# Optimization experiments

Measured on AMD Instinct MI355X. Metric: run time of the kernel, lower is better.

Reference implementation:

```python
import jax, jax.numpy as jnp
import numpy as np

N_U = 8192
N_C = 8192
D_IN = 32
D_HID = 32  # hidden_dim == output_dim (required by the concat->Linear shape)


def _glorot(key, fan_in, fan_out):
    r = np.sqrt(6.0 / (fan_in + fan_out)).astype(np.float32)
    return jax.random.uniform(key, (fan_in, fan_out), jnp.float32, -r, r)


def setup_inputs() -> dict:
    key = jax.random.key(0)
    ks = jax.random.split(key, 12)
    X_U = jax.random.normal(ks[0], (N_U, D_IN), jnp.float32)
    X_C = jax.random.normal(ks[1], (N_C, D_IN), jnp.float32)
    adj_uu = jax.random.uniform(ks[2], (N_U, N_U), jnp.float32)
    adj_uc = jax.random.uniform(ks[3], (N_U, N_C), jnp.float32)
    adj_cc = jax.random.uniform(ks[4], (N_C, N_C), jnp.float32)
    weight_s = _glorot(ks[5], D_IN, D_HID)          # GCN_S.weight (shared for uu and cc)
    proj_u = _glorot(ks[6], D_IN, D_HID)            # GCN_C.projection_u
    proj_c = _glorot(ks[7], D_IN, D_HID)            # GCN_C.projection_c (unused in fwd math)
    weight_c = _glorot(ks[8], D_HID, D_HID)         # GCN_C.weight
    W_lin = jax.random.normal(ks[9], (D_IN + D_HID, D_HID), jnp.float32) * 0.05  # Linear, no bias
    a_vec = jax.random.normal(ks[10], (D_HID, 1), jnp.float32) * 0.05            # attention vector
    return {"X_U": X_U, "X_C": X_C, "adj_uu": adj_uu, "adj_uc": adj_uc, "adj_cc": adj_cc,
            "weight_s": weight_s, "proj_u": proj_u, "proj_c": proj_c,
            "weight_c": weight_c, "W_lin": W_lin, "a_vec": a_vec}


def gcn_s(adj, x, w):
    # D^-1/2 A D^-1/2 (X W), with D = 1 + rowsum(A); expressed as broadcast scaling
    dinv = jax.lax.rsqrt(1.0 + jnp.sum(adj, axis=1))  # [N]
    support = x @ w                                    # [N, d]
    return dinv[:, None] * (adj @ (dinv[:, None] * support))


def gcn_c(adj, x_u, p_u, w):
    # Du^-1/2 A Dc^-1/2 ((X_U P_u) W); projected_c is computed but unused upstream
    du = jax.lax.rsqrt(jnp.sum(adj, axis=1))  # [N_u]
    dc = jax.lax.rsqrt(jnp.sum(adj, axis=0))  # [N_c]
    support = (x_u @ p_u) @ w                  # [N_u, d]
    return du[:, None] * (adj @ (dc[:, None] * support))  # wait: see note below


def gcn_c_correct(adj, x_u, p_u, w):
    # norm_adj = diag(du) @ adj @ diag(dc)  -> [N_u, N_c]; output = norm_adj @ support ([N_u,d])
    # Actually original multiplies [N_u,N_c] norm_adj by support built from X_U [N_u,d]:
    # this only typechecks when N_u == N_c (as in the repo's usage). We keep that math.
    du = jax.lax.rsqrt(jnp.sum(adj, axis=1))
    dc = jax.lax.rsqrt(jnp.sum(adj, axis=0))
    support = (x_u @ p_u) @ w
    return du[:, None] * (adj @ (dc[:, None] * support))


def reference(X_U, X_C, adj_uu, adj_uc, adj_cc, weight_s, proj_u, proj_c, weight_c, W_lin, a_vec):
    node_embed_u = gcn_s(adj_uu, X_U, weight_s)            # [N_u, d]
    node_embed_c1 = gcn_s(adj_cc, X_C, weight_s)           # [N_c, d]
    node_embed_c2 = gcn_c_correct(adj_uc, X_U, proj_u, weight_c)  # [N_c, d]

    a_tau_1 = jax.nn.relu(jnp.concatenate([node_embed_c1, X_C], axis=-1) @ W_lin) @ a_vec  # [N_c,1]
    a_tau_2 = jax.nn.relu(jnp.concatenate([node_embed_c2, X_C], axis=-1) @ W_lin) @ a_vec  # [N_c,1]
    e_tau = jax.nn.softmax(jnp.concatenate([a_tau_1, a_tau_2], axis=1), axis=1)            # [N_c,2]

    Y_c = e_tau[:, 0:1] * node_embed_c1
    Y_u = e_tau[:, 1:2] * node_embed_c2
    node_embed_c = Y_c + Y_u
    return (node_embed_u, node_embed_c, Y_c, Y_u)
```

## Files before the change

kernel.cpp:

```cpp
#include <hip/hip_runtime.h>
#include <hip/hip_bf16.h>

#define N_NODES 8192

typedef __attribute__((ext_vector_type(8))) short short8;
typedef __attribute__((ext_vector_type(8))) unsigned short ushort8;
typedef __attribute__((ext_vector_type(4))) unsigned short ushort4v;
typedef __attribute__((ext_vector_type(4))) float floatx4;

__device__ inline unsigned short f2bf(float f) {
  unsigned int u = __float_as_uint(f);
  u = (u + 0x7FFFu + ((u >> 16) & 1u)) >> 16;
  return (unsigned short)u;
}

__device__ inline float waveSum(float s) {
#pragma unroll
  for (int off = 32; off >= 1; off >>= 1) s += __shfl_xor(s, off, 64);
  return s;
}

__device__ inline void acc4(float4& a, const float4 b) {
  a.x += b.x; a.y += b.y; a.z += b.z; a.w += b.w;
}
__device__ inline float hsum4(const float4 v) { return v.x + v.y + v.z + v.w; }

__device__ inline short8 cvt8(const float4 lo, const float4 hi) {
  short8 r;
  r[0] = (short)f2bf(lo.x); r[1] = (short)f2bf(lo.y);
  r[2] = (short)f2bf(lo.z); r[3] = (short)f2bf(lo.w);
  r[4] = (short)f2bf(hi.x); r[5] = (short)f2bf(hi.y);
  r[6] = (short)f2bf(hi.z); r[7] = (short)f2bf(hi.w);
  return r;
}

__global__ __launch_bounds__(256) void k_degree(
    const float* __restrict__ a_uu, const float* __restrict__ a_cc,
    const float* __restrict__ a_uc,
    float* __restrict__ dinv_uu, float* __restrict__ dinv_cc,
    float* __restrict__ du, float* __restrict__ cs) {
  const int y = blockIdx.y;
  const float* A = (y == 0) ? a_uu : (y == 1) ? a_cc : a_uc;
  const bool uc = (y == 2);
  int t = threadIdx.x, w = t >> 6, l = t & 63;
  long r0 = (long)blockIdx.x * 32;
  __shared__ float rp_lds[32][4];

  float4 colacc[8];
#pragma unroll
  for (int m = 0; m < 8; ++m) colacc[m] = (float4){0.f, 0.f, 0.f, 0.f};

#pragma unroll 2
  for (int r = 0; r < 32; ++r) {
    const float* rowp = A + (r0 + r) * N_NODES + 4 * t;
    float4 v[8];
#pragma unroll
    for (int m = 0; m < 8; ++m) v[m] = *(const float4*)(rowp + 1024 * m);
    float rp = 0.f;
#pragma unroll
    for (int m = 0; m < 8; ++m) {
      rp += hsum4(v[m]);
      if (uc) acc4(colacc[m], v[m]);
    }
    rp = waveSum(rp);
    if (l == 0) rp_lds[r][w] = rp;
  }
  __syncthreads();
  if (t < 32) {
    float s = rp_lds[t][0] + rp_lds[t][1] + rp_lds[t][2] + rp_lds[t][3];
    if (y == 0) dinv_uu[r0 + t] = rsqrtf(1.0f + s);
    else if (y == 1) dinv_cc[r0 + t] = rsqrtf(1.0f + s);
    else du[r0 + t] = rsqrtf(s);
  }
  if (uc) {
#pragma unroll
    for (int m = 0; m < 8; ++m) {
      float* cp = cs + 4 * t + 1024 * m;
      atomicAdd(cp + 0, colacc[m].x);
      atomicAdd(cp + 1, colacc[m].y);
      atomicAdd(cp + 2, colacc[m].z);
      atomicAdd(cp + 3, colacc[m].w);
    }
  }
}

__global__ __launch_bounds__(256) void k_finalize(const float* __restrict__ cs,
                                                  float* __restrict__ dc) {
  int i = blockIdx.x * 256 + threadIdx.x;
  dc[i] = rsqrtf(cs[i]);
}

__global__ void k_projw(const float* __restrict__ proj_u,
                        const float* __restrict__ weight_c, float* __restrict__ P) {
  int t = threadIdx.x;
  int i = t >> 5, j = t & 31;
  float s = 0.f;
#pragma unroll
  for (int k = 0; k < 32; ++k) s += proj_u[i * 32 + k] * weight_c[k * 32 + j];
  P[t] = s;
}

__global__ __launch_bounds__(256) void k_support(
    const float* __restrict__ X_U, const float* __restrict__ X_C,
    const float* __restrict__ weight_s, const float* __restrict__ P,
    const float* __restrict__ dinv_uu, const float* __restrict__ dinv_cc,
    const float* __restrict__ dc,
    unsigned short* __restrict__ bt_uu, unsigned short* __restrict__ bt_cc,
    unsigned short* __restrict__ bt_uc) {
  int m = blockIdx.y;
  const float* X = (m == 1) ? X_C : X_U;
  const float* W = (m == 2) ? P : weight_s;
  const float* dv = (m == 0) ? dinv_uu : (m == 1) ? dinv_cc : dc;
  unsigned short* bt = (m == 0) ? bt_uu : (m == 1) ? bt_cc : bt_uc;
  __shared__ float Wl[32][32];
  __shared__ float Xl[8][32];
  int t = threadIdx.x;
#pragma unroll
  for (int i = 0; i < 4; ++i) {
    int idx = t + 256 * i;
    Wl[idx >> 5][idx & 31] = W[idx];
  }
  int r = t >> 5, n = t & 31;
  int j0 = blockIdx.x * 8;
  Xl[r][n] = X[(long)(j0 + r) * 32 + n];
  __syncthreads();
  float s = 0.f;
#pragma unroll
  for (int k = 0; k < 32; ++k) s += Xl[r][k] * Wl[k][n];
  s *= dv[j0 + r];
  bt[(long)n * N_NODES + j0 + r] = f2bf(s);
}

__global__ __launch_bounds__(256) void k_gemm(
    const float* __restrict__ adj_uu, const float* __restrict__ adj_cc,
    const float* __restrict__ adj_uc,
    const unsigned short* __restrict__ bt_uu, const unsigned short* __restrict__ bt_cc,
    const unsigned short* __restrict__ bt_uc,
    const float* __restrict__ dinv_uu, const float* __restrict__ dinv_cc,
    const float* __restrict__ du,
    float* __restrict__ out_u, float* __restrict__ c1, float* __restrict__ c2) {
  int m = blockIdx.y;
  const float* adj = (m == 0) ? adj_uu : (m == 1) ? adj_cc : adj_uc;
  const unsigned short* bt = (m == 0) ? bt_uu : (m == 1) ? bt_cc : bt_uc;
  const float* dsc = (m == 0) ? dinv_uu : (m == 1) ? dinv_cc : du;
  float* outp = (m == 0) ? out_u : (m == 1) ? c1 : c2;

  int t = threadIdx.x;
  int w = t >> 6, l = t & 63;
  int mh = w & 1, nh = w >> 1;
  long r0 = (long)blockIdx.x * 32;

  const float* pa = adj + (r0 + 16 * mh + (l & 15)) * (long)N_NODES + ((l >> 4) * 8);
  const short* pb = (const short*)bt + (long)(16 * nh + (l & 15)) * N_NODES + ((l >> 4) * 8);

  floatx4 acc = {0.f, 0.f, 0.f, 0.f};

  float4 a0[8]; short8 b0[4];
  float4 a1[8]; short8 b1[4];

#define LOAD_TILE(A_, B_, OFF)                                        \
  _Pragma("unroll") for (int kk = 0; kk < 4; ++kk) {                  \
    A_[2 * kk]     = *(const float4*)(pa + (OFF) + kk * 32);          \
    A_[2 * kk + 1] = *(const float4*)(pa + (OFF) + kk * 32 + 4);      \
    B_[kk]         = *(const short8*)(pb + (OFF) + kk * 32);          \
  }

#define COMPUTE_TILE(A_, B_)                                          \
  _Pragma("unroll") for (int kk = 0; kk < 4; ++kk) {                  \
    short8 af = cvt8(A_[2 * kk], A_[2 * kk + 1]);                     \
    acc = __builtin_amdgcn_mfma_f32_16x16x32_bf16(af, B_[kk], acc, 0, 0, 0); \
  }

  LOAD_TILE(a0, b0, 0)
  for (int step = 0; step < 64; step += 2) {
    LOAD_TILE(a1, b1, (step + 1) * 128)
    COMPUTE_TILE(a0, b0)
    if (step + 2 < 64) {
      LOAD_TILE(a0, b0, (step + 2) * 128)
    }
    COMPUTE_TILE(a1, b1)
  }
#undef LOAD_TILE
#undef COMPUTE_TILE

  int mrow = (int)r0 + 16 * mh + ((l >> 4) << 2);
  int ncol = 16 * nh + (l & 15);
#pragma unroll
  for (int r = 0; r < 4; ++r) {
    float sc = dsc[mrow + r];
    outp[(long)(mrow + r) * 32 + ncol] = sc * acc[r];
  }
}

__global__ __launch_bounds__(256) void k_epilogue(
    const float* __restrict__ c1, const float* __restrict__ c2,
    const float* __restrict__ X_C, const float* __restrict__ W_lin,
    const float* __restrict__ a_vec, float* __restrict__ out) {
  __shared__ float Wl[64][32];
  __shared__ float al[32];
  int t = threadIdx.x;
#pragma unroll
  for (int i = 0; i < 8; ++i) {
    int idx = t + 256 * i;
    Wl[idx >> 5][idx & 31] = W_lin[idx];
  }
  if (t < 32) al[t] = a_vec[t];
  int g = t >> 5, n = t & 31;
  long row = (long)blockIdx.x * 8 + g;
  __syncthreads();
  float h1 = c1[row * 32 + n];
  float h2 = c2[row * 32 + n];
  float xv = X_C[row * 32 + n];
  float s1 = 0.f, s2 = 0.f, sx = 0.f;
#pragma unroll
  for (int k = 0; k < 32; ++k) {
    float h1k = __shfl(h1, k, 32);
    float h2k = __shfl(h2, k, 32);
    float xk = __shfl(xv, k, 32);
    float w0 = Wl[k][n], w1 = Wl[32 + k][n];
    s1 += h1k * w0;
    s2 += h2k * w0;
    sx += xk * w1;
  }
  float t1 = fmaxf(s1 + sx, 0.f) * al[n];
  float t2 = fmaxf(s2 + sx, 0.f) * al[n];
#pragma unroll
  for (int off = 16; off >= 1; off >>= 1) {
    t1 += __shfl_xor(t1, off, 32);
    t2 += __shfl_xor(t2, off, 32);
  }
  float mx = fmaxf(t1, t2);
  float e1 = expf(t1 - mx), e2 = expf(t2 - mx);
  float inv = 1.0f / (e1 + e2);
  float w1w = e1 * inv, w2w = e2 * inv;
  float yc = w1w * h1, yu = w2w * h2;
  long o = row * 32 + n;
  out[262144 + o] = yc + yu;
  out[524288 + o] = yc;
  out[786432 + o] = yu;
}

extern "C" void kernel_launch(void* const* d_in, const int* in_sizes, int n_in,
                              void* d_out, int out_size, void* d_ws, size_t ws_size,
                              hipStream_t stream) {
  (void)in_sizes; (void)n_in; (void)out_size; (void)ws_size;
  const float* X_U = (const float*)d_in[0];
  const float* X_C = (const float*)d_in[1];
  const float* adj_uu = (const float*)d_in[2];
  const float* adj_uc = (const float*)d_in[3];
  const float* adj_cc = (const float*)d_in[4];
  const float* weight_s = (const float*)d_in[5];
  const float* proj_u = (const float*)d_in[6];
  const float* weight_c = (const float*)d_in[8];
  const float* W_lin = (const float*)d_in[9];
  const float* a_vec = (const float*)d_in[10];
  float* out = (float*)d_out;

  char* ws = (char*)d_ws;
  auto alloc = [&](size_t bytes) {
    char* p = ws;
    ws += (bytes + 255) & ~(size_t)255;
    return p;
  };
  float* dinv_uu = (float*)alloc(8192 * 4);
  float* dinv_cc = (float*)alloc(8192 * 4);
  float* du = (float*)alloc(8192 * 4);
  float* dc = (float*)alloc(8192 * 4);
  float* cs = (float*)alloc(8192 * 4);
  float* P = (float*)alloc(1024 * 4);
  float* c1 = (float*)alloc((size_t)262144 * 4);
  float* c2 = (float*)alloc((size_t)262144 * 4);
  unsigned short* bt_uu = (unsigned short*)alloc((size_t)262144 * 2);
  unsigned short* bt_cc = (unsigned short*)alloc((size_t)262144 * 2);
  unsigned short* bt_uc = (unsigned short*)alloc((size_t)262144 * 2);

  hipMemsetAsync(cs, 0, 8192 * 4, stream);
  hipLaunchKernelGGL(k_degree, dim3(256, 3), dim3(256), 0, stream,
                     adj_uu, adj_cc, adj_uc, dinv_uu, dinv_cc, du, cs);
  hipLaunchKernelGGL(k_finalize, dim3(32), dim3(256), 0, stream, cs, dc);
  hipLaunchKernelGGL(k_projw, dim3(1), dim3(1024), 0, stream, proj_u, weight_c, P);
  hipLaunchKernelGGL(k_support, dim3(1024, 3), dim3(256), 0, stream,
                     X_U, X_C, weight_s, P, dinv_uu, dinv_cc, dc, bt_uu, bt_cc, bt_uc);
  hipLaunchKernelGGL(k_gemm, dim3(256, 3), dim3(256), 0, stream,
                     adj_uu, adj_cc, adj_uc, bt_uu, bt_cc, bt_uc,
                     dinv_uu, dinv_cc, du, out, c1, c2);
  hipLaunchKernelGGL(k_epilogue, dim3(1024), dim3(256), 0, stream,
                     c1, c2, X_C, W_lin, a_vec, out);
}
```

Before: 960.1 us.

## Stage GEMM tiles through LDS with single bf16 conversion; shrink degree blocks

The GEMM kernel now loads A and B tiles cooperatively into shared memory, converting each adjacency element to bf16 once, and the MFMA operands are read from LDS. Before, each wave loaded and converted its own A fragment, so every A element was converted twice across the two N-halves. The new loop uses two barriers per step and only a register prefetch, in place of the earlier two-tile register double buffering. The degree kernel processes 16 rows per block, doubles the grid, defers the wave reductions until after all loads, and requests an occupancy bound to expose more memory parallelism.

After: 1.181 ms. 1.23x slower.

```diff
diff --git a/kernel.cpp b/kernel.cpp
--- a/kernel.cpp
+++ b/kernel.cpp
@@ -25,16 +25,7 @@
 }
 __device__ inline float hsum4(const float4 v) { return v.x + v.y + v.z + v.w; }
 
-__device__ inline short8 cvt8(const float4 lo, const float4 hi) {
-  short8 r;
-  r[0] = (short)f2bf(lo.x); r[1] = (short)f2bf(lo.y);
-  r[2] = (short)f2bf(lo.z); r[3] = (short)f2bf(lo.w);
-  r[4] = (short)f2bf(hi.x); r[5] = (short)f2bf(hi.y);
-  r[6] = (short)f2bf(hi.z); r[7] = (short)f2bf(hi.w);
-  return r;
-}
-
-__global__ __launch_bounds__(256) void k_degree(
+__global__ __launch_bounds__(256, 4) void k_degree(
     const float* __restrict__ a_uu, const float* __restrict__ a_cc,
     const float* __restrict__ a_uc,
     float* __restrict__ dinv_uu, float* __restrict__ dinv_cc,
@@ -43,31 +34,35 @@
   const float* A = (y == 0) ? a_uu : (y == 1) ? a_cc : a_uc;
   const bool uc = (y == 2);
   int t = threadIdx.x, w = t >> 6, l = t & 63;
-  long r0 = (long)blockIdx.x * 32;
-  __shared__ float rp_lds[32][4];
+  long r0 = (long)blockIdx.x * 16;
+  __shared__ float xw[16][4];
 
   float4 colacc[8];
 #pragma unroll
   for (int m = 0; m < 8; ++m) colacc[m] = (float4){0.f, 0.f, 0.f, 0.f};
 
-#pragma unroll 2
-  for (int r = 0; r < 32; ++r) {
+  float rp[16];
+#pragma unroll
+  for (int r = 0; r < 16; ++r) {
     const float* rowp = A + (r0 + r) * N_NODES + 4 * t;
-    float4 v[8];
-#pragma unroll
-    for (int m = 0; m < 8; ++m) v[m] = *(const float4*)(rowp + 1024 * m);
-    float rp = 0.f;
+    float s = 0.f;
 #pragma unroll
     for (int m = 0; m < 8; ++m) {
-      rp += hsum4(v[m]);
-      if (uc) acc4(colacc[m], v[m]);
+      float4 v = *(const float4*)(rowp + 1024 * m);
+      s += hsum4(v);
+      if (uc) acc4(colacc[m], v);
     }
-    rp = waveSum(rp);
-    if (l == 0) rp_lds[r][w] = rp;
+    rp[r] = s;
+  }
+
+#pragma unroll
+  for (int r = 0; r < 16; ++r) {
+    float s = waveSum(rp[r]);
+    if (l == 0) xw[r][w] = s;
   }
   __syncthreads();
-  if (t < 32) {
-    float s = rp_lds[t][0] + rp_lds[t][1] + rp_lds[t][2] + rp_lds[t][3];
+  if (t < 16) {
+    float s = xw[t][0] + xw[t][1] + xw[t][2] + xw[t][3];
     if (y == 0) dinv_uu[r0 + t] = rsqrtf(1.0f + s);
     else if (y == 1) dinv_cc[r0 + t] = rsqrtf(1.0f + s);
     else du[r0 + t] = rsqrtf(s);
@@ -145,43 +140,61 @@
   const float* dsc = (m == 0) ? dinv_uu : (m == 1) ? dinv_cc : du;
   float* outp = (m == 0) ? out_u : (m == 1) ? c1 : c2;
 
+  __shared__ unsigned short As[32][136];
+  __shared__ unsigned short Bs[32][136];
+
   int t = threadIdx.x;
   int w = t >> 6, l = t & 63;
   int mh = w & 1, nh = w >> 1;
   long r0 = (long)blockIdx.x * 32;
 
-  const float* pa = adj + (r0 + 16 * mh + (l & 15)) * (long)N_NODES + ((l >> 4) * 8);
-  const short* pb = (const short*)bt + (long)(16 * nh + (l & 15)) * N_NODES + ((l >> 4) * 8);
+  int ar = t >> 3, ac = (t & 7) * 4;
+  int bn = t >> 3, bk = (t & 7) * 8;
+
+  const float* ap = adj + (r0 + ar) * N_NODES + ac;
+  const unsigned short* bp = bt + (long)bn * N_NODES + bk;
+
+  float4 a0 = *(const float4*)(ap + 0);
+  float4 a1 = *(const float4*)(ap + 32);
+  float4 a2 = *(const float4*)(ap + 64);
+  float4 a3 = *(const float4*)(ap + 96);
+  ushort8 b0 = *(const ushort8*)(bp + 0);
+  ushort8 b1 = *(const ushort8*)(bp + 64);
 
   floatx4 acc = {0.f, 0.f, 0.f, 0.f};
 
-  float4 a0[8]; short8 b0[4];
-  float4 a1[8]; short8 b1[4];
-
-#define LOAD_TILE(A_, B_, OFF)                                        \
-  _Pragma("unroll") for (int kk = 0; kk < 4; ++kk) {                  \
-    A_[2 * kk]     = *(const float4*)(pa + (OFF) + kk * 32);          \
-    A_[2 * kk + 1] = *(const float4*)(pa + (OFF) + kk * 32 + 4);      \
-    B_[kk]         = *(const short8*)(pb + (OFF) + kk * 32);          \
-  }
-
-#define COMPUTE_TILE(A_, B_)                                          \
-  _Pragma("unroll") for (int kk = 0; kk < 4; ++kk) {                  \
-    short8 af = cvt8(A_[2 * kk], A_[2 * kk + 1]);                     \
-    acc = __builtin_amdgcn_mfma_f32_16x16x32_bf16(af, B_[kk], acc, 0, 0, 0); \
-  }
-
-  LOAD_TILE(a0, b0, 0)
-  for (int step = 0; step < 64; step += 2) {
-    LOAD_TILE(a1, b1, (step + 1) * 128)
-    COMPUTE_TILE(a0, b0)
-    if (step + 2 < 64) {
-      LOAD_TILE(a0, b0, (step + 2) * 128)
+  for (int step = 0; step < 64; ++step) {
+    ushort4v q;
+    q.x = f2bf(a0.x); q.y = f2bf(a0.y); q.z = f2bf(a0.z); q.w = f2bf(a0.w);
+    *(ushort4v*)&As[ar][ac + 0] = q;
+    q.x = f2bf(a1.x); q.y = f2bf(a1.y); q.z = f2bf(a1.z); q.w = f2bf(a1.w);
+    *(ushort4v*)&As[ar][ac + 32] = q;
+    q.x = f2bf(a2.x); q.y = f2bf(a2.y); q.z = f2bf(a2.z); q.w = f2bf(a2.w);
+    *(ushort4v*)&As[ar][ac + 64] = q;
+    q.x = f2bf(a3.x); q.y = f2bf(a3.y); q.z = f2bf(a3.z); q.w = f2bf(a3.w);
+    *(ushort4v*)&As[ar][ac + 96] = q;
+    *(ushort8*)&Bs[bn][bk + 0] = b0;
+    *(ushort8*)&Bs[bn][bk + 64] = b1;
+    __syncthreads();
+
+    if (step < 63) {
+      ap += 128; bp += 128;
+      a0 = *(const float4*)(ap + 0);
+      a1 = *(const float4*)(ap + 32);
+      a2 = *(const float4*)(ap + 64);
+      a3 = *(const float4*)(ap + 96);
+      b0 = *(const ushort8*)(bp + 0);
+      b1 = *(const ushort8*)(bp + 64);
     }
-    COMPUTE_TILE(a1, b1)
-  }
-#undef LOAD_TILE
-#undef COMPUTE_TILE
+
+#pragma unroll
+    for (int kk = 0; kk < 4; ++kk) {
+      short8 af = *(const short8*)&As[16 * mh + (l & 15)][kk * 32 + (l >> 4) * 8];
+      short8 bf = *(const short8*)&Bs[16 * nh + (l & 15)][kk * 32 + (l >> 4) * 8];
+      acc = __builtin_amdgcn_mfma_f32_16x16x32_bf16(af, bf, acc, 0, 0, 0);
+    }
+    __syncthreads();
+  }
 
   int mrow = (int)r0 + 16 * mh + ((l >> 4) << 2);
   int ncol = 16 * nh + (l & 15);
@@ -275,7 +288,7 @@
   unsigned short* bt_uc = (unsigned short*)alloc((size_t)262144 * 2);
 
   hipMemsetAsync(cs, 0, 8192 * 4, stream);
-  hipLaunchKernelGGL(k_degree, dim3(256, 3), dim3(256), 0, stream,
+  hipLaunchKernelGGL(k_degree, dim3(512, 3), dim3(256), 0, stream,
                      adj_uu, adj_cc, adj_uc, dinv_uu, dinv_cc, du, cs);
   hipLaunchKernelGGL(k_finalize, dim3(32), dim3(256), 0, stream, cs, dc);
   hipLaunchKernelGGL(k_projw, dim3(1), dim3(1024), 0, stream, proj_u, weight_c, P);
```
